# Optimization experiments

Hardware: AMD Instinct MI355X
Metric: run time of the kernel (lower is better)

Reference implementation:

```python
import jax, jax.numpy as jnp
import numpy as np

P_DROP = 0.25
DROP_KEY_SEED = 42  # fixed seed makes dropout deterministic for baseline comparison


def setup_inputs() -> dict:
    key = jax.random.key(0)
    k1, k2, k3, k4 = jax.random.split(key, 4)
    B, S, D, DV = 16, 2048, 64, 512
    x1 = jax.random.normal(k1, (B, S, D), dtype=jnp.float32)   # queries [B,S,64]
    m = jax.random.normal(k2, (D, DV), dtype=jnp.float32)      # [64,512]
    n = jax.random.normal(k3, (S, DV), dtype=jnp.float32)      # [S,512]
    q = jax.random.normal(k4, (S, DV), dtype=jnp.float32)      # values [S,512]
    return {"x1": x1, "m": m, "n": n, "q": q}


def reference(x1, m, n, q):
    scale = jnp.float32(1.0 / 64.0)  # hard-coded in original (not 1/sqrt(d))
    kT = jnp.matmul(m, n.T)                        # matmul5: [64, S]
    scores = jnp.matmul(x1, kT) * scale            # [B, S, S]
    probs = jax.nn.softmax(scores, axis=-1)        # softmax over last dim
    keep = jax.random.bernoulli(jax.random.key(DROP_KEY_SEED), 1.0 - P_DROP, probs.shape)
    probs = jnp.where(keep, probs / (1.0 - P_DROP), jnp.float32(0.0))  # dropout (train mode)
    return jnp.matmul(probs, q)                    # [B, S, DV]
```

## Files before the change

### kernel.cpp

```cpp
#include <hip/hip_runtime.h>


typedef short  s8v __attribute__((ext_vector_type(8)));
typedef float  f4v __attribute__((ext_vector_type(4)));

__device__ __forceinline__ unsigned short f2bf(float f) {
  unsigned int u = __float_as_uint(f);
  u += 0x7fffu + ((u >> 16) & 1u);
  return (unsigned short)(u >> 16);
}
__device__ __forceinline__ float bf2f(unsigned short h) {
  return __uint_as_float(((unsigned int)h) << 16);
}

__device__ __forceinline__ unsigned int rotl(unsigned int x, unsigned int r) {
  return __builtin_amdgcn_alignbit(x, x, 32u - r);
}

__device__ __forceinline__ unsigned int jax_bits(unsigned int idx) {
  const unsigned int K0 = 0u, K1 = 42u, K2 = 0x1BD11BDAu ^ K0 ^ K1;
  unsigned int x0 = 0u, x1 = idx;
  x0 += K0; x1 += K1;
#define TF_R(r) { x0 += x1; x1 = rotl(x1, r); x1 ^= x0; }
  TF_R(13) TF_R(15) TF_R(26) TF_R(6)
  x0 += K1; x1 += K2 + 1u;
  TF_R(17) TF_R(29) TF_R(16) TF_R(24)
  x0 += K2; x1 += K0 + 2u;
  TF_R(13) TF_R(15) TF_R(26) TF_R(6)
  x0 += K0; x1 += K1 + 3u;
  TF_R(17) TF_R(29) TF_R(16) TF_R(24)
  x0 += K1; x1 += K2 + 4u;
  TF_R(13) TF_R(15) TF_R(26) TF_R(6)
  x0 += K2; x1 += K0 + 5u;
#undef TF_R
  return x0 ^ x1;
}

__device__ __forceinline__ f4v mfma16(s8v a, s8v b, f4v c) {
  return __builtin_amdgcn_mfma_f32_16x16x32_bf16(a, b, c, 0, 0, 0);
}

__global__ void prep_all(const float* __restrict__ x1, const float* __restrict__ q,
                         const float* __restrict__ m, const float* __restrict__ nmat,
                         unsigned short* __restrict__ Xhi, unsigned short* __restrict__ qT,
                         unsigned short* __restrict__ Khi, unsigned short* __restrict__ Klo) {
  const int blk = blockIdx.x;
  const int t = threadIdx.x;
  if (blk < 512) {
    __shared__ float Lm[64][68];
    const int s = blk * 4 + (t >> 6);
    const int d = t & 63;
    float a0 = 0.f, a1 = 0.f, a2 = 0.f, a3 = 0.f;
    for (int ch = 0; ch < 8; ++ch) {
      const int dv0 = ch * 64;
      __syncthreads();
#pragma unroll
      for (int k = 0; k < 4; ++k) {
        const int fi = t + k * 256;
        const int row = fi >> 4, c4 = fi & 15;
        *(float4*)&Lm[row][c4 * 4] =
            *(const float4*)&m[(size_t)row * 512 + dv0 + c4 * 4];
      }
      __syncthreads();
      const float4* nv = (const float4*)&nmat[(size_t)s * 512 + dv0];
#pragma unroll
      for (int j4 = 0; j4 < 16; ++j4) {
        const float4 nf = nv[j4];
        const float4 mf = *(const float4*)&Lm[d][j4 * 4];
        a0 = fmaf(mf.x, nf.x, a0); a1 = fmaf(mf.y, nf.y, a1);
        a2 = fmaf(mf.z, nf.z, a2); a3 = fmaf(mf.w, nf.w, a3);
      }
    }
    const float kv = ((a0 + a1) + (a2 + a3)) * (1.44269504088896340736f / 64.0f);
    const unsigned short h = f2bf(kv);
    Khi[s * 64 + d] = h;
    Klo[s * 64 + d] = f2bf(kv - bf2f(h));
  } else if (blk < 1536) {
    const int i = ((blk - 512) * 256 + t) * 8;
    float4 a = *(const float4*)&x1[i];
    float4 b = *(const float4*)&x1[i + 4];
    ushort4 o0, o1;
    o0.x = f2bf(a.x); o0.y = f2bf(a.y); o0.z = f2bf(a.z); o0.w = f2bf(a.w);
    o1.x = f2bf(b.x); o1.y = f2bf(b.y); o1.z = f2bf(b.z); o1.w = f2bf(b.w);
    *(ushort4*)&Xhi[i] = o0;
    *(ushort4*)&Xhi[i + 4] = o1;
  } else {
    __shared__ unsigned short tile[64][65];
    const int bb = blk - 1536;
    const int s0 = (bb >> 3) * 64;
    const int d0 = (bb & 7) * 64;
#pragma unroll
    for (int k = 0; k < 16; ++k) {
      int lin = t + k * 256;
      int r = lin >> 6, c = lin & 63;
      tile[c][r] = f2bf(q[(size_t)(s0 + r) * 512 + d0 + c]);
    }
    __syncthreads();
#pragma unroll
    for (int k = 0; k < 16; ++k) {
      int lin = t + k * 256;
      int rr = lin >> 6, cc = lin & 63;
      qT[(size_t)(d0 + rr) * 2048 + s0 + cc] = tile[rr][cc];
    }
  }
}

__global__ __launch_bounds__(512, 4) void attn_main(
    const unsigned short* __restrict__ Xhi,
    const unsigned short* __restrict__ Khi, const unsigned short* __restrict__ Klo,
    const unsigned short* __restrict__ qT, float* __restrict__ out) {
  __shared__ unsigned short Xs[64][72];
  __shared__ unsigned short Ps[2][64][136];
  __shared__ float rsum[8][64];

  const int tid  = threadIdx.x;
  const int wave = tid >> 6;
  const int lane = tid & 63;
  const int l15  = lane & 15;
  const int quad = lane >> 4;

  const int b    = blockIdx.x >> 5;
  const int row0 = (blockIdx.x & 31) * 64;

  {
    const int r = tid >> 3, c8 = (tid & 7) * 8;
    *(uint4*)&Xs[r][c8] =
        *(const uint4*)&Xhi[((size_t)(b * 2048 + row0 + r)) * 64 + c8];
  }

  const unsigned short* __restrict__ khp = Khi + ((wave * 16 + l15) * 64 + quad * 8);
  const unsigned short* __restrict__ klp = Klo + ((wave * 16 + l15) * 64 + quad * 8);
  const unsigned short* __restrict__ qvp = qT + ((wave * 64 + l15) * 2048 + quad * 8);

  s8v Kh0 = *(const s8v*)(khp);
  s8v Kh1 = *(const s8v*)(khp + 32);
  s8v Kl0 = *(const s8v*)(klp);
  s8v Kl1 = *(const s8v*)(klp + 32);

  f4v acc[4][4];
#pragma unroll
  for (int mt = 0; mt < 4; ++mt)
#pragma unroll
    for (int nt = 0; nt < 4; ++nt) acc[mt][nt] = f4v{0.f, 0.f, 0.f, 0.f};
  float rs[4] = {0.f, 0.f, 0.f, 0.f};

  const unsigned int idxl =
      ((unsigned int)(b * 2048 + row0 + l15)) * 2048u +
      (unsigned int)(wave * 16 + quad * 4);

  __syncthreads();

  for (int it = 0; it < 16; ++it) {
    const int kt = it * 128;
    unsigned short (*Pb)[136] = Ps[it & 1];

#pragma unroll
    for (int nt = 0; nt < 4; ++nt) {
      const s8v Xb0 = *(const s8v*)&Xs[nt * 16 + l15][quad * 8];
      const s8v Xb1 = *(const s8v*)&Xs[nt * 16 + l15][quad * 8 + 32];
      f4v c = {0.f, 0.f, 0.f, 0.f};
      c = mfma16(Kh0, Xb0, c);  c = mfma16(Kh1, Xb1, c);
      c = mfma16(Kl0, Xb0, c);  c = mfma16(Kl1, Xb1, c);
      const unsigned int idx0 = idxl + (unsigned int)(nt * 32768 + kt);
      float p[4];
#pragma unroll
      for (int r = 0; r < 4; ++r) {
        float e = exp2f(c[r]);
        rs[nt] += e;
        const unsigned int bits = jax_bits(idx0 + r);
        p[r] = (bits < 0xC0000000u) ? e : 0.0f;
      }
      unsigned int p01, p23;
      asm("v_cvt_pk_bf16_f32 %0, %1, %2" : "=v"(p01) : "v"(p[0]), "v"(p[1]));
      asm("v_cvt_pk_bf16_f32 %0, %1, %2" : "=v"(p23) : "v"(p[2]), "v"(p[3]));
      *(uint2*)&Pb[nt * 16 + l15][wave * 16 + quad * 4] = make_uint2(p01, p23);
    }

    if (it < 15) {
      const int ko = (it + 1) * 8192;
      Kh0 = *(const s8v*)(khp + ko);
      Kh1 = *(const s8v*)(khp + ko + 32);
      Kl0 = *(const s8v*)(klp + ko);
      Kl1 = *(const s8v*)(klp + ko + 32);
    }

    __syncthreads();

#pragma unroll
    for (int ks = 0; ks < 4; ++ks) {
      s8v Va[4];
#pragma unroll
      for (int mt = 0; mt < 4; ++mt)
        Va[mt] = *(const s8v*)(qvp + mt * (16 * 2048) + kt + ks * 32);
      __builtin_amdgcn_s_setprio(1);
#pragma unroll
      for (int nt = 0; nt < 4; ++nt) {
        const s8v Pf = *(const s8v*)&Pb[nt * 16 + l15][ks * 32 + quad * 8];
#pragma unroll
        for (int mt = 0; mt < 4; ++mt) acc[mt][nt] = mfma16(Va[mt], Pf, acc[mt][nt]);
      }
      __builtin_amdgcn_s_setprio(0);
    }
  }

#pragma unroll
  for (int nt = 0; nt < 4; ++nt) {
    float v = rs[nt];
    v += __shfl_xor(v, 16);
    v += __shfl_xor(v, 32);
    if (quad == 0) rsum[wave][nt * 16 + l15] = v;
  }
  __syncthreads();

#pragma unroll
  for (int nt = 0; nt < 4; ++nt) {
    const int rloc = nt * 16 + l15;
    float tot = 0.f;
#pragma unroll
    for (int w2 = 0; w2 < 8; ++w2) tot += rsum[w2][rloc];
    const float inv = 1.0f / (0.75f * tot);
    const size_t base = ((size_t)(b * 2048 + row0 + rloc)) * 512 + wave * 64;
#pragma unroll
    for (int mt = 0; mt < 4; ++mt) {
      f4v v = acc[mt][nt];
      v[0] *= inv; v[1] *= inv; v[2] *= inv; v[3] *= inv;
      *(f4v*)&out[base + mt * 16 + quad * 4] = v;
    }
  }
}

extern "C" void kernel_launch(void* const* d_in, const int* in_sizes, int n_in,
                              void* d_out, int out_size, void* d_ws, size_t ws_size,
                              hipStream_t stream) {
  (void)in_sizes; (void)n_in; (void)out_size; (void)ws_size;
  const float* x1 = (const float*)d_in[0];
  const float* m  = (const float*)d_in[1];
  const float* n  = (const float*)d_in[2];
  const float* q  = (const float*)d_in[3];
  float* out = (float*)d_out;

  char* ws = (char*)d_ws;
  unsigned short* Khi = (unsigned short*)(ws);
  unsigned short* Klo = (unsigned short*)(ws + 262144);
  unsigned short* Xhi = (unsigned short*)(ws + 524288);
  unsigned short* qT  = (unsigned short*)(ws + 4718592);

  prep_all<<<1792, 256, 0, stream>>>(x1, q, m, n, Xhi, qT, Khi, Klo);
  attn_main<<<512, 512, 0, stream>>>(Xhi, Khi, Klo, qT, out);
}
```

Before: 312.3 us.

## Fuse x1 bf16 conversion into attention kernel and software-pipeline K/V loads

Removes the separate x1-to-bf16 pass from the prep kernel; the attention kernel now loads fp32 x1 and converts it while filling shared memory. This avoids writing and re-reading a bf16 copy of x1. The loop is also restructured so the next K fragments are fetched before the exp/dropout work, the first V fragments are loaded before the barrier, and the next V fragments are prefetched after each MFMA group. The syncthreads is replaced by an explicit lgkmcnt wait plus s_barrier and a sched_barrier. This adds register pressure and an unconditional redundant K load on the last iteration.

```diff
diff --git a/kernel.cpp b/kernel.cpp
--- a/kernel.cpp
+++ b/kernel.cpp
@@ -40,9 +40,9 @@
   return __builtin_amdgcn_mfma_f32_16x16x32_bf16(a, b, c, 0, 0, 0);
 }
 
-__global__ void prep_all(const float* __restrict__ x1, const float* __restrict__ q,
+__global__ void prep_all(const float* __restrict__ q,
                          const float* __restrict__ m, const float* __restrict__ nmat,
-                         unsigned short* __restrict__ Xhi, unsigned short* __restrict__ qT,
+                         unsigned short* __restrict__ qT,
                          unsigned short* __restrict__ Khi, unsigned short* __restrict__ Klo) {
   const int blk = blockIdx.x;
   const int t = threadIdx.x;
@@ -75,18 +75,9 @@
     const unsigned short h = f2bf(kv);
     Khi[s * 64 + d] = h;
     Klo[s * 64 + d] = f2bf(kv - bf2f(h));
-  } else if (blk < 1536) {
-    const int i = ((blk - 512) * 256 + t) * 8;
-    float4 a = *(const float4*)&x1[i];
-    float4 b = *(const float4*)&x1[i + 4];
-    ushort4 o0, o1;
-    o0.x = f2bf(a.x); o0.y = f2bf(a.y); o0.z = f2bf(a.z); o0.w = f2bf(a.w);
-    o1.x = f2bf(b.x); o1.y = f2bf(b.y); o1.z = f2bf(b.z); o1.w = f2bf(b.w);
-    *(ushort4*)&Xhi[i] = o0;
-    *(ushort4*)&Xhi[i + 4] = o1;
   } else {
     __shared__ unsigned short tile[64][65];
-    const int bb = blk - 1536;
+    const int bb = blk - 512;
     const int s0 = (bb >> 3) * 64;
     const int d0 = (bb & 7) * 64;
 #pragma unroll
@@ -106,7 +97,7 @@
 }
 
 __global__ __launch_bounds__(512, 4) void attn_main(
-    const unsigned short* __restrict__ Xhi,
+    const float* __restrict__ x1,
     const unsigned short* __restrict__ Khi, const unsigned short* __restrict__ Klo,
     const unsigned short* __restrict__ qT, float* __restrict__ out) {
   __shared__ unsigned short Xs[64][72];
@@ -124,19 +115,22 @@
 
   {
     const int r = tid >> 3, c8 = (tid & 7) * 8;
-    *(uint4*)&Xs[r][c8] =
-        *(const uint4*)&Xhi[((size_t)(b * 2048 + row0 + r)) * 64 + c8];
+    const float* xp = &x1[((size_t)(b * 2048 + row0 + r)) * 64 + c8];
+    float4 a = *(const float4*)xp;
+    float4 bb = *(const float4*)(xp + 4);
+    uint4 w;
+    w.x = ((unsigned)f2bf(a.x)) | ((unsigned)f2bf(a.y) << 16);
+    w.y = ((unsigned)f2bf(a.z)) | ((unsigned)f2bf(a.w) << 16);
+    w.z = ((unsigned)f2bf(bb.x)) | ((unsigned)f2bf(bb.y) << 16);
+    w.w = ((unsigned)f2bf(bb.z)) | ((unsigned)f2bf(bb.w) << 16);
+    *(uint4*)&Xs[r][c8] = w;
   }
 
   const unsigned short* __restrict__ khp = Khi + ((wave * 16 + l15) * 64 + quad * 8);
   const unsigned short* __restrict__ klp = Klo + ((wave * 16 + l15) * 64 + quad * 8);
   const unsigned short* __restrict__ qvp = qT + ((wave * 64 + l15) * 2048 + quad * 8);
 
-  s8v Kh0 = *(const s8v*)(khp);
-  s8v Kh1 = *(const s8v*)(khp + 32);
-  s8v Kl0 = *(const s8v*)(klp);
-  s8v Kl1 = *(const s8v*)(klp + 32);
-
+  s8v Kh0, Kh1, Kl0, Kl1;
   f4v acc[4][4];
 #pragma unroll
   for (int mt = 0; mt < 4; ++mt)
@@ -148,24 +142,44 @@
       ((unsigned int)(b * 2048 + row0 + l15)) * 2048u +
       (unsigned int)(wave * 16 + quad * 4);
 
+  {
+    Kh0 = *(const s8v*)(khp);
+    Kh1 = *(const s8v*)(khp + 32);
+    Kl0 = *(const s8v*)(klp);
+    Kl1 = *(const s8v*)(klp + 32);
+  }
   __syncthreads();
 
   for (int it = 0; it < 16; ++it) {
     const int kt = it * 128;
     unsigned short (*Pb)[136] = Ps[it & 1];
 
+    f4v c[4];
 #pragma unroll
     for (int nt = 0; nt < 4; ++nt) {
       const s8v Xb0 = *(const s8v*)&Xs[nt * 16 + l15][quad * 8];
       const s8v Xb1 = *(const s8v*)&Xs[nt * 16 + l15][quad * 8 + 32];
-      f4v c = {0.f, 0.f, 0.f, 0.f};
-      c = mfma16(Kh0, Xb0, c);  c = mfma16(Kh1, Xb1, c);
-      c = mfma16(Kl0, Xb0, c);  c = mfma16(Kl1, Xb1, c);
+      f4v cc = {0.f, 0.f, 0.f, 0.f};
+      cc = mfma16(Kh0, Xb0, cc);  cc = mfma16(Kh1, Xb1, cc);
+      cc = mfma16(Kl0, Xb0, cc);  cc = mfma16(Kl1, Xb1, cc);
+      c[nt] = cc;
+    }
+
+    {
+      const int kon = (it + 1 < 16 ? it + 1 : 15) * 8192;
+      Kh0 = *(const s8v*)(khp + kon);
+      Kh1 = *(const s8v*)(khp + kon + 32);
+      Kl0 = *(const s8v*)(klp + kon);
+      Kl1 = *(const s8v*)(klp + kon + 32);
+    }
+
+#pragma unroll
+    for (int nt = 0; nt < 4; ++nt) {
       const unsigned int idx0 = idxl + (unsigned int)(nt * 32768 + kt);
       float p[4];
 #pragma unroll
       for (int r = 0; r < 4; ++r) {
-        float e = exp2f(c[r]);
+        float e = exp2f(c[nt][r]);
         rs[nt] += e;
         const unsigned int bits = jax_bits(idx0 + r);
         p[r] = (bits < 0xC0000000u) ? e : 0.0f;
@@ -176,22 +190,17 @@
       *(uint2*)&Pb[nt * 16 + l15][wave * 16 + quad * 4] = make_uint2(p01, p23);
     }
 
-    if (it < 15) {
-      const int ko = (it + 1) * 8192;
-      Kh0 = *(const s8v*)(khp + ko);
-      Kh1 = *(const s8v*)(khp + ko + 32);
-      Kl0 = *(const s8v*)(klp + ko);
-      Kl1 = *(const s8v*)(klp + ko + 32);
-    }
-
-    __syncthreads();
+    s8v Va[4];
+#pragma unroll
+    for (int mt = 0; mt < 4; ++mt)
+      Va[mt] = *(const s8v*)(qvp + mt * (16 * 2048) + kt);
+
+    asm volatile("s_waitcnt lgkmcnt(0)" ::: "memory");
+    __builtin_amdgcn_s_barrier();
+    __builtin_amdgcn_sched_barrier(0);
 
 #pragma unroll
     for (int ks = 0; ks < 4; ++ks) {
-      s8v Va[4];
-#pragma unroll
-      for (int mt = 0; mt < 4; ++mt)
-        Va[mt] = *(const s8v*)(qvp + mt * (16 * 2048) + kt + ks * 32);
       __builtin_amdgcn_s_setprio(1);
 #pragma unroll
       for (int nt = 0; nt < 4; ++nt) {
@@ -200,6 +209,11 @@
         for (int mt = 0; mt < 4; ++mt) acc[mt][nt] = mfma16(Va[mt], Pf, acc[mt][nt]);
       }
       __builtin_amdgcn_s_setprio(0);
+      if (ks < 3) {
+#pragma unroll
+        for (int mt = 0; mt < 4; ++mt)
+          Va[mt] = *(const s8v*)(qvp + mt * (16 * 2048) + kt + (ks + 1) * 32);
+      }
     }
   }
 
@@ -242,9 +256,8 @@
   char* ws = (char*)d_ws;
   unsigned short* Khi = (unsigned short*)(ws);
   unsigned short* Klo = (unsigned short*)(ws + 262144);
-  unsigned short* Xhi = (unsigned short*)(ws + 524288);
-  unsigned short* qT  = (unsigned short*)(ws + 4718592);
-
-  prep_all<<<1792, 256, 0, stream>>>(x1, q, m, n, Xhi, qT, Khi, Klo);
-  attn_main<<<512, 512, 0, stream>>>(Xhi, Khi, Klo, qT, out);
-}
+  unsigned short* qT  = (unsigned short*)(ws + 524288);
+
+  prep_all<<<768, 256, 0, stream>>>(q, m, n, qT, Khi, Klo);
+  attn_main<<<512, 512, 0, stream>>>(x1, Khi, Klo, qT, out);
+}
```

After: 288.6 us. -7.6%, faster.
